# Kernel tuning notes

Hardware: AMD Instinct MI355X
Metric: run time of the kernel (lower is better)

The kernel has to match this reference:

```python
import jax, jax.numpy as jnp
import numpy as np

B, S, HID = 1, 4096, 2048
NH, NKV, HD = 16, 4, 128
BLK, LOCAL, GNB, STRIDE = 64, 4, 2, 4
ROT = 64  # head_dim * rope_partial_rotary_factor(0.5), already even
SCALE = HD ** -0.5
NEG = -1e9


def _block_select(nb):
    """Static local+global key-block selection per query block (mirrors _select_key_blocks)."""
    sels = []
    for bi in range(nb):
        local = list(range(max(0, bi - LOCAL + 1), bi + 1))
        gc = list(range(0, bi + 1, STRIDE))
        if len(gc) > GNB:
            gc = gc[-GNB:]
        if 0 not in gc:
            gc = [0] + gc
        idx = sorted(set(local + gc))
        sels.append([i for i in idx if 0 <= i < nb and i <= bi])
    m = max(len(s) for s in sels)
    idx = np.zeros((nb, m), np.int32)
    valid = np.zeros((nb, m), bool)
    for i, s in enumerate(sels):
        idx[i, :len(s)] = s
        valid[i, :len(s)] = True
    return jnp.asarray(idx), jnp.asarray(valid)


def _rot_half(x):
    h = x.shape[-1] // 2
    return jnp.concatenate([-x[..., h:], x[..., :h]], axis=-1)


def setup_inputs() -> dict:
    key = jax.random.key(0)
    ks = jax.random.split(key, 8)
    w = lambda k, shp: (jax.random.normal(k, shp, jnp.float32) * 0.02)
    return {
        "hidden": jax.random.normal(ks[0], (B, S, HID), jnp.float32),
        "cos": jax.random.uniform(ks[1], (B, S, ROT), jnp.float32, -1.0, 1.0),
        "sin": jax.random.uniform(ks[2], (B, S, ROT), jnp.float32, -1.0, 1.0),
        "Wq": w(ks[3], (HID, NH * HD)),
        "Wk": w(ks[4], (HID, NKV * HD)),
        "Wv": w(ks[5], (HID, NKV * HD)),
        "Wo": w(ks[6], (NH * HD, HID)),
        "attn_mask": jnp.ones((B, S), jnp.float32),
    }


def reference(hidden, cos, sin, Wq, Wk, Wv, Wo, attn_mask):
    b_, s_, _ = hidden.shape
    q = (hidden @ Wq).reshape(b_, s_, NH, HD).transpose(0, 2, 1, 3)   # [B,H,S,d]
    k = (hidden @ Wk).reshape(b_, s_, NKV, HD).transpose(0, 2, 1, 3)  # [B,Hkv,S,d]
    v = (hidden @ Wv).reshape(b_, s_, NKV, HD).transpose(0, 2, 1, 3)

    # partial RoPE on first ROT channels
    c = cos[:, None, :, :]
    sn = sin[:, None, :, :]
    q1, q2 = q[..., :ROT], q[..., ROT:]
    k1, k2 = k[..., :ROT], k[..., ROT:]
    q = jnp.concatenate([q1 * c + _rot_half(q1) * sn, q2], axis=-1)
    k = jnp.concatenate([k1 * c + _rot_half(k1) * sn, k2], axis=-1)

    # repeat_kv (GQA expand: each kv head repeated contiguously)
    rep = NH // NKV
    k = jnp.repeat(k, rep, axis=1)
    v = jnp.repeat(v, rep, axis=1)

    nb = s_ // BLK  # S chosen divisible by BLK (pad_len == 0)
    qb = q.reshape(b_, NH, nb, BLK, HD)
    kb = k.reshape(b_, NH, nb, BLK, HD)
    vb = v.reshape(b_, NH, nb, BLK, HD)

    idx, valid = _block_select(nb)  # [nb, M]
    m = idx.shape[1]
    ksel = kb[:, :, idx]  # [B,H,nb,M,BLK,d]
    vsel = vb[:, :, idx]

    scores = jnp.einsum('bhnqd,bhnmkd->bhnqmk',
                        qb.astype(jnp.float32), ksel.astype(jnp.float32)) * SCALE
    # key-validity (padding) mask, additive as in original
    key_valid = attn_mask.reshape(b_, nb, BLK)
    kvm = key_valid[:, idx]  # [B,nb,M,BLK]
    scores = scores + (1.0 - kvm[:, None, :, None, :, :]) * NEG
    # invalid (padded) selected slots
    scores = jnp.where(valid[None, None, :, None, :, None], scores, NEG)
    # intra-block causal mask on the diagonal block
    intra = jnp.triu(jnp.ones((BLK, BLK), bool), 1)                    # [q,k]
    same = idx == jnp.arange(nb)[:, None]                              # [nb,M]
    diag = same[:, None, :, None] & intra[None, :, None, :]            # [nb,q,M,k]
    scores = jnp.where(diag[None, None], NEG, scores)

    probs = jax.nn.softmax(scores.reshape(b_, NH, nb, BLK, m * BLK), axis=-1)
    vflat = vsel.reshape(b_, NH, nb, m * BLK, HD)
    out = jnp.einsum('bhnqe,bhned->bhnqd', probs.astype(v.dtype), vflat)
    out = out.reshape(b_, NH, s_, HD).transpose(0, 2, 1, 3).reshape(b_, s_, NH * HD)
    return out @ Wo
```

## Files before the change

### kernel.cpp

```cpp
#include <hip/hip_runtime.h>
#include <hip/hip_bf16.h>


typedef short short8 __attribute__((ext_vector_type(8)));
typedef float f32x4 __attribute__((ext_vector_type(4)));

#define NEGV   (-1.0e9f)
#define SCALE  (0.08838834764831845f)

__device__ __forceinline__ void gload16(const void* g, void* l) {
  __builtin_amdgcn_global_load_lds(
      (const __attribute__((address_space(1))) unsigned int*)g,
      (__attribute__((address_space(3))) unsigned int*)l, 16, 0, 0);
}

__device__ __forceinline__ float bf2f(short s) {
  union { unsigned u; float f; } c;
  c.u = ((unsigned)(unsigned short)s) << 16;
  return c.f;
}

__device__ __forceinline__ short f2bf_s(float f) {
  __hip_bfloat16 b = __float2bfloat16(f);
  short s;
  __builtin_memcpy(&s, &b, 2);
  return s;
}

__global__ void conv_hidden(const float* __restrict__ H, __hip_bfloat16* __restrict__ X) {
  size_t t = (size_t)blockIdx.x * 256 + threadIdx.x;
  float4 v = *(const float4*)(H + t * 4);
  __hip_bfloat16* o = X + t * 4;
  o[0] = __float2bfloat16(v.x); o[1] = __float2bfloat16(v.y);
  o[2] = __float2bfloat16(v.z); o[3] = __float2bfloat16(v.w);
}

__global__ void transpose_f32_to_bf16(const float* __restrict__ src,
                                      __hip_bfloat16* __restrict__ dst,
                                      int R, int C) {
  __shared__ __hip_bfloat16 tile[64][73];
  int r0 = blockIdx.x * 64, c0 = blockIdx.y * 64;
  int c = threadIdx.x & 63, rq = threadIdx.x >> 6;
#pragma unroll
  for (int i = 0; i < 16; ++i) {
    int r = i * 4 + rq;
    tile[r][c] = __float2bfloat16(src[(size_t)(r0 + r) * C + c0 + c]);
  }
  __syncthreads();
#pragma unroll
  for (int i = 0; i < 16; ++i) {
    int cc = i * 4 + rq;
    dst[(size_t)(c0 + cc) * R + r0 + c] = tile[c][cc];
  }
}

__global__ void transpose_v(const __hip_bfloat16* __restrict__ QKV,
                            __hip_bfloat16* __restrict__ Vt) {
  __shared__ __hip_bfloat16 tile[64][73];
  int s0 = blockIdx.x * 64, c0 = blockIdx.y * 64;
  int c = threadIdx.x & 63, rq = threadIdx.x >> 6;
#pragma unroll
  for (int i = 0; i < 16; ++i) {
    int r = i * 4 + rq;
    tile[r][c] = QKV[(size_t)(s0 + r) * 3072 + 2560 + c0 + c];
  }
  __syncthreads();
#pragma unroll
  for (int i = 0; i < 16; ++i) {
    int cc = i * 4 + rq;
    Vt[(size_t)(c0 + cc) * 4096 + s0 + c] = tile[c][cc];
  }
}

__global__ void rope_qk(const __hip_bfloat16* __restrict__ QKV, const float* __restrict__ cosb,
                        const float* __restrict__ sinb, __hip_bfloat16* __restrict__ Qb,
                        __hip_bfloat16* __restrict__ Kb) {
  size_t t = (size_t)blockIdx.x * 256 + threadIdx.x;
  const size_t QT = (size_t)4096 * 256;
  int s, cg; const __hip_bfloat16* row; __hip_bfloat16* dst;
  if (t < QT) {
    s = (int)(t >> 8); cg = (int)(t & 255) * 8;
    row = QKV + (size_t)s * 3072;
    dst = Qb + (size_t)s * 2048 + cg;
  } else {
    size_t tk = t - QT;
    s = (int)(tk >> 6); cg = (int)(tk & 63) * 8;
    row = QKV + (size_t)s * 3072 + 2048;
    dst = Kb + (size_t)s * 512 + cg;
  }
  int d = cg & 127;
  short8 v = *(const short8*)(row + cg);
  if (d < 64) {
    short8 p = *(const short8*)(row + cg + (d < 32 ? 32 : -32));
    float sg = (d < 32) ? -1.f : 1.f;
    const float* cp = cosb + (size_t)s * 64 + d;
    const float* sp = sinb + (size_t)s * 64 + d;
    float4 c0 = *(const float4*)cp, c1 = *(const float4*)(cp + 4);
    float4 s0 = *(const float4*)sp, s1 = *(const float4*)(sp + 4);
    float cs[8] = {c0.x, c0.y, c0.z, c0.w, c1.x, c1.y, c1.z, c1.w};
    float sn[8] = {s0.x, s0.y, s0.z, s0.w, s1.x, s1.y, s1.z, s1.w};
    short8 o;
#pragma unroll
    for (int i = 0; i < 8; ++i) {
      float r = bf2f(v[i]) * cs[i] + sg * bf2f(p[i]) * sn[i];
      o[i] = f2bf_s(r);
    }
    *(short8*)dst = o;
  } else {
    *(short8*)dst = v;
  }
}

template <typename OutT>
__global__ __launch_bounds__(256) void gemm_bt(
    const __hip_bfloat16* __restrict__ A, const __hip_bfloat16* __restrict__ Bt,
    OutT* __restrict__ C, int M, int N, int K) {
  const int tid = threadIdx.x;
  const int wave = tid >> 6, lane = tid & 63;
  const int l15 = lane & 15, lg = lane >> 4;
  const int bm = blockIdx.x, bn = blockIdx.y;
  const int wm = wave >> 1, wn = wave & 1;

  __shared__ __hip_bfloat16 As[128 * 64];
  __shared__ __hip_bfloat16 Bs[128 * 64];

  f32x4 acc[4][4] = {};
  const int lrow = lane >> 3;
  const int lslot = lane & 7;
  const int scol = (lslot ^ lrow) * 8;
  const size_t abase = (size_t)bm * 128 * K;
  const size_t bbase = (size_t)bn * 128 * K;
  const int r3 = l15 & 7;

  for (int k0 = 0; k0 < K; k0 += 64) {
#pragma unroll
    for (int i = 0; i < 4; ++i) {
      int seg = i * 4 + wave;
      int row = seg * 8 + lrow;
      gload16(A + abase + (size_t)row * K + k0 + scol, &As[seg * 512]);
      gload16(Bt + bbase + (size_t)row * K + k0 + scol, &Bs[seg * 512]);
    }
    __syncthreads();
#pragma unroll
    for (int ks = 0; ks < 2; ++ks) {
      const int slot = (ks * 4 + lg) ^ r3;
      short8 af[4], bf[4];
#pragma unroll
      for (int mi = 0; mi < 4; ++mi)
        af[mi] = *(const short8*)&As[(wm * 64 + mi * 16 + l15) * 64 + slot * 8];
#pragma unroll
      for (int ni = 0; ni < 4; ++ni)
        bf[ni] = *(const short8*)&Bs[(wn * 64 + ni * 16 + l15) * 64 + slot * 8];
#pragma unroll
      for (int mi = 0; mi < 4; ++mi)
#pragma unroll
        for (int ni = 0; ni < 4; ++ni)
          acc[mi][ni] = __builtin_amdgcn_mfma_f32_16x16x32_bf16(af[mi], bf[ni], acc[mi][ni], 0, 0, 0);
    }
    __syncthreads();
  }
#pragma unroll
  for (int mi = 0; mi < 4; ++mi)
#pragma unroll
    for (int ni = 0; ni < 4; ++ni) {
      int row = bm * 128 + wm * 64 + mi * 16 + lg * 4;
      int col = bn * 128 + wn * 64 + ni * 16 + l15;
#pragma unroll
      for (int r = 0; r < 4; ++r) {
        float v = acc[mi][ni][r];
        if constexpr (__hip_internal::is_same<OutT, float>::value)
          C[(size_t)(row + r) * N + col] = v;
        else
          C[(size_t)(row + r) * N + col] = __float2bfloat16(v);
      }
    }
}

__global__ __launch_bounds__(256, 2) void attn_kernel(
    const __hip_bfloat16* __restrict__ Qb,
    const __hip_bfloat16* __restrict__ Kb,
    const __hip_bfloat16* __restrict__ Vt,
    const float* __restrict__ amask,
    __hip_bfloat16* __restrict__ AO)
{
  const int bid = blockIdx.x;
  const int h = bid & 15;
  const int bi = bid >> 4;
  const int kvh = h >> 2;
  const int tid = threadIdx.x;
  const int wave = tid >> 6, lane = tid & 63;
  const int l15 = lane & 15, lg = lane >> 4;

  int sel[6]; int nsel = 0;
  {
    int gtop = bi >> 2;
    for (int j = 0; j <= bi; ++j) {
      bool pick = (j == 0) || (j >= bi - 3) || (((j & 3) == 0) && ((j >> 2) >= gtop - 1));
      if (pick && nsel < 6) sel[nsel++] = j;
    }
  }

  __shared__ __hip_bfloat16 kvs[128 * 72];
  __shared__ __hip_bfloat16 Pb[64 * 72];

  short8 qf[4];
  {
    const __hip_bfloat16* qbase =
        Qb + (size_t)(bi * 64 + wave * 16 + l15) * 2048 + h * 128 + lg * 8;
#pragma unroll
    for (int ks = 0; ks < 4; ++ks) qf[ks] = *(const short8*)(qbase + ks * 32);
  }

  f32x4 sc[6][4] = {};
#pragma unroll
  for (int j = 0; j < 6; ++j) {
    if (j < nsel) {
      int kb = sel[j];
#pragma unroll
      for (int i = 0; i < 4; ++i) {
        int e = (i * 256 + tid) * 8;
        int r = e >> 7, c = e & 127;
        short8 v = *(const short8*)(Kb + (size_t)(kb * 64 + r) * 512 + kvh * 128 + c);
        *(short8*)&kvs[r * 136 + c] = v;
      }
      __syncthreads();
#pragma unroll
      for (int nf = 0; nf < 4; ++nf)
#pragma unroll
        for (int ks = 0; ks < 4; ++ks) {
          short8 bfr = *(const short8*)&kvs[(nf * 16 + l15) * 136 + ks * 32 + lg * 8];
          sc[j][nf] = __builtin_amdgcn_mfma_f32_16x16x32_bf16(qf[ks], bfr, sc[j][nf], 0, 0, 0);
        }
      __syncthreads();
    }
  }

  float rowmax[4] = {-3.0e38f, -3.0e38f, -3.0e38f, -3.0e38f};
#pragma unroll
  for (int j = 0; j < 6; ++j) {
    if (j >= nsel) continue;
    int kb = sel[j];
#pragma unroll
    for (int nf = 0; nf < 4; ++nf) {
      int keyg = kb * 64 + nf * 16 + l15;
      float mterm = (1.0f - amask[keyg]) * NEGV;
      int keyl = nf * 16 + l15;
#pragma unroll
      for (int r = 0; r < 4; ++r) {
        float s = sc[j][nf][r] * SCALE + mterm;
        if (kb == bi) {
          int qrow = wave * 16 + lg * 4 + r;
          if (keyl > qrow) s = NEGV;
        }
        sc[j][nf][r] = s;
        rowmax[r] = fmaxf(rowmax[r], s);
      }
    }
  }
#pragma unroll
  for (int r = 0; r < 4; ++r) {
    float v = rowmax[r];
    v = fmaxf(v, __shfl_xor(v, 1)); v = fmaxf(v, __shfl_xor(v, 2));
    v = fmaxf(v, __shfl_xor(v, 4)); v = fmaxf(v, __shfl_xor(v, 8));
    rowmax[r] = v;
  }
  float rinv[4] = {0.f, 0.f, 0.f, 0.f};
#pragma unroll
  for (int j = 0; j < 6; ++j) {
    if (j >= nsel) continue;
#pragma unroll
    for (int nf = 0; nf < 4; ++nf)
#pragma unroll
      for (int r = 0; r < 4; ++r) {
        float p = __expf(sc[j][nf][r] - rowmax[r]);
        sc[j][nf][r] = p;
        rinv[r] += p;
      }
  }
#pragma unroll
  for (int r = 0; r < 4; ++r) {
    float v = rinv[r];
    v += __shfl_xor(v, 1); v += __shfl_xor(v, 2);
    v += __shfl_xor(v, 4); v += __shfl_xor(v, 8);
    rinv[r] = 1.0f / v;
  }

  f32x4 oacc[8] = {};
#pragma unroll
  for (int j = 0; j < 6; ++j) {
    if (j < nsel) {
      int kb = sel[j];
#pragma unroll
      for (int nf = 0; nf < 4; ++nf)
#pragma unroll
        for (int r = 0; r < 4; ++r) {
          int qrow = wave * 16 + lg * 4 + r;
          Pb[qrow * 72 + nf * 16 + l15] = __float2bfloat16(sc[j][nf][r] * rinv[r]);
        }
#pragma unroll
      for (int i = 0; i < 4; ++i) {
        int e = (i * 256 + tid) * 8;
        int d = e >> 6, c = e & 63;
        short8 v = *(const short8*)(Vt + (size_t)(kvh * 128 + d) * 4096 + kb * 64 + c);
        *(short8*)&kvs[d * 72 + c] = v;
      }
      __syncthreads();
#pragma unroll
      for (int ks = 0; ks < 2; ++ks) {
        short8 pa = *(const short8*)&Pb[(wave * 16 + l15) * 72 + ks * 32 + lg * 8];
#pragma unroll
        for (int df = 0; df < 8; ++df) {
          short8 vb = *(const short8*)&kvs[(df * 16 + l15) * 72 + ks * 32 + lg * 8];
          oacc[df] = __builtin_amdgcn_mfma_f32_16x16x32_bf16(pa, vb, oacc[df], 0, 0, 0);
        }
      }
      __syncthreads();
    }
  }

#pragma unroll
  for (int df = 0; df < 8; ++df)
#pragma unroll
    for (int r = 0; r < 4; ++r) {
      int qrow = bi * 64 + wave * 16 + lg * 4 + r;
      AO[(size_t)qrow * 2048 + h * 128 + df * 16 + l15] = __float2bfloat16(oacc[df][r]);
    }
}

extern "C" void kernel_launch(void* const* d_in, const int* in_sizes, int n_in,
                              void* d_out, int out_size, void* d_ws, size_t ws_size,
                              hipStream_t stream) {
  const float* hidden = (const float*)d_in[0];
  const float* cosb   = (const float*)d_in[1];
  const float* sinb   = (const float*)d_in[2];
  const float* Wq     = (const float*)d_in[3];
  const float* Wk     = (const float*)d_in[4];
  const float* Wv     = (const float*)d_in[5];
  const float* Wo     = (const float*)d_in[6];
  const float* amask  = (const float*)d_in[7];

  char* ws = (char*)d_ws;
  __hip_bfloat16* Xb   = (__hip_bfloat16*)(ws);
  __hip_bfloat16* Wt   = (__hip_bfloat16*)(ws + 16777216);
  __hip_bfloat16* Wot  = (__hip_bfloat16*)(ws + 29360128);
  __hip_bfloat16* QKVb = (__hip_bfloat16*)(ws + 37748736);
  __hip_bfloat16* Qb   = (__hip_bfloat16*)(ws + 62914560);
  __hip_bfloat16* Kb   = (__hip_bfloat16*)(ws + 79691776);
  __hip_bfloat16* Vt   = (__hip_bfloat16*)(ws + 83886080);
  __hip_bfloat16* AO   = Xb;

  conv_hidden<<<8192, 256, 0, stream>>>(hidden, Xb);
  transpose_f32_to_bf16<<<dim3(32, 32), 256, 0, stream>>>(Wq, Wt, 2048, 2048);
  transpose_f32_to_bf16<<<dim3(32, 8),  256, 0, stream>>>(Wk, Wt + (size_t)2048 * 2048, 2048, 512);
  transpose_f32_to_bf16<<<dim3(32, 8),  256, 0, stream>>>(Wv, Wt + (size_t)2560 * 2048, 2048, 512);
  transpose_f32_to_bf16<<<dim3(32, 32), 256, 0, stream>>>(Wo, Wot, 2048, 2048);

  gemm_bt<__hip_bfloat16><<<dim3(32, 24), 256, 0, stream>>>(Xb, Wt, QKVb, 4096, 3072, 2048);

  rope_qk<<<5120, 256, 0, stream>>>(QKVb, cosb, sinb, Qb, Kb);
  transpose_v<<<dim3(64, 8), 256, 0, stream>>>(QKVb, Vt);

  attn_kernel<<<1024, 256, 0, stream>>>(Qb, Kb, Vt, amask, AO);

  gemm_bt<float><<<dim3(32, 16), 256, 0, stream>>>(AO, Wot, (float*)d_out, 4096, 2048, 2048);
}
```

Measured before the change: 182.0 us.

## Fuse RoPE and V transpose into QKV GEMM epilogue

The QKV projection GEMM now applies partial RoPE to Q and K tiles directly from its accumulators and writes V transposed, so the separate rope_qk and transpose_v kernels and the intermediate QKV buffer go away. This removes two kernel launches and a full write and re-read of the 4096x3072 intermediate. In exchange, the epilogue does strided per-element cos/sin loads and scattered transposed stores from the GEMM. RoPE is also now applied to fp32 accumulators before bf16 rounding, which changes numerics slightly.

```diff
diff --git a/kernel.cpp b/kernel.cpp
--- a/kernel.cpp
+++ b/kernel.cpp
@@ -3,7 +3,8 @@
 
 
 typedef short short8 __attribute__((ext_vector_type(8)));
-typedef float f32x4 __attribute__((ext_vector_type(4)));
+typedef short s16x4  __attribute__((ext_vector_type(4)));
+typedef float f32x4  __attribute__((ext_vector_type(4)));
 
 #define NEGV   (-1.0e9f)
 #define SCALE  (0.08838834764831845f)
@@ -54,67 +55,12 @@
   }
 }
 
-__global__ void transpose_v(const __hip_bfloat16* __restrict__ QKV,
-                            __hip_bfloat16* __restrict__ Vt) {
-  __shared__ __hip_bfloat16 tile[64][73];
-  int s0 = blockIdx.x * 64, c0 = blockIdx.y * 64;
-  int c = threadIdx.x & 63, rq = threadIdx.x >> 6;
-#pragma unroll
-  for (int i = 0; i < 16; ++i) {
-    int r = i * 4 + rq;
-    tile[r][c] = QKV[(size_t)(s0 + r) * 3072 + 2560 + c0 + c];
-  }
-  __syncthreads();
-#pragma unroll
-  for (int i = 0; i < 16; ++i) {
-    int cc = i * 4 + rq;
-    Vt[(size_t)(c0 + cc) * 4096 + s0 + c] = tile[c][cc];
-  }
-}
-
-__global__ void rope_qk(const __hip_bfloat16* __restrict__ QKV, const float* __restrict__ cosb,
-                        const float* __restrict__ sinb, __hip_bfloat16* __restrict__ Qb,
-                        __hip_bfloat16* __restrict__ Kb) {
-  size_t t = (size_t)blockIdx.x * 256 + threadIdx.x;
-  const size_t QT = (size_t)4096 * 256;
-  int s, cg; const __hip_bfloat16* row; __hip_bfloat16* dst;
-  if (t < QT) {
-    s = (int)(t >> 8); cg = (int)(t & 255) * 8;
-    row = QKV + (size_t)s * 3072;
-    dst = Qb + (size_t)s * 2048 + cg;
-  } else {
-    size_t tk = t - QT;
-    s = (int)(tk >> 6); cg = (int)(tk & 63) * 8;
-    row = QKV + (size_t)s * 3072 + 2048;
-    dst = Kb + (size_t)s * 512 + cg;
-  }
-  int d = cg & 127;
-  short8 v = *(const short8*)(row + cg);
-  if (d < 64) {
-    short8 p = *(const short8*)(row + cg + (d < 32 ? 32 : -32));
-    float sg = (d < 32) ? -1.f : 1.f;
-    const float* cp = cosb + (size_t)s * 64 + d;
-    const float* sp = sinb + (size_t)s * 64 + d;
-    float4 c0 = *(const float4*)cp, c1 = *(const float4*)(cp + 4);
-    float4 s0 = *(const float4*)sp, s1 = *(const float4*)(sp + 4);
-    float cs[8] = {c0.x, c0.y, c0.z, c0.w, c1.x, c1.y, c1.z, c1.w};
-    float sn[8] = {s0.x, s0.y, s0.z, s0.w, s1.x, s1.y, s1.z, s1.w};
-    short8 o;
-#pragma unroll
-    for (int i = 0; i < 8; ++i) {
-      float r = bf2f(v[i]) * cs[i] + sg * bf2f(p[i]) * sn[i];
-      o[i] = f2bf_s(r);
-    }
-    *(short8*)dst = o;
-  } else {
-    *(short8*)dst = v;
-  }
-}
-
-template <typename OutT>
-__global__ __launch_bounds__(256) void gemm_bt(
+__global__ __launch_bounds__(256) void gemm_qkv(
     const __hip_bfloat16* __restrict__ A, const __hip_bfloat16* __restrict__ Bt,
-    OutT* __restrict__ C, int M, int N, int K) {
+    const float* __restrict__ cosb, const float* __restrict__ sinb,
+    __hip_bfloat16* __restrict__ Qb, __hip_bfloat16* __restrict__ Kb,
+    __hip_bfloat16* __restrict__ Vt) {
+  const int K = 2048;
   const int tid = threadIdx.x;
   const int wave = tid >> 6, lane = tid & 63;
   const int l15 = lane & 15, lg = lane >> 4;
@@ -159,6 +105,94 @@
     }
     __syncthreads();
   }
+
+  const int srow0 = bm * 128 + wm * 64;
+  if (bn < 20) {
+    __hip_bfloat16* dst; int ld;
+    if (bn < 16) { dst = Qb + (size_t)bn * 128;        ld = 2048; }
+    else         { dst = Kb + (size_t)(bn - 16) * 128; ld = 512;  }
+#pragma unroll
+    for (int mi = 0; mi < 4; ++mi)
+#pragma unroll
+      for (int ni = 0; ni < 4; ++ni) {
+        int dcol = wn * 64 + ni * 16 + l15;
+        int srow = srow0 + mi * 16 + lg * 4;
+#pragma unroll
+        for (int r = 0; r < 4; ++r) {
+          float v = acc[mi][ni][r];
+          if (wn == 0) {
+            int s = srow + r;
+            float cv = cosb[(size_t)s * 64 + dcol];
+            float sv = sinb[(size_t)s * 64 + dcol];
+            float pv = acc[mi][ni ^ 2][r];
+            v = v * cv + (ni < 2 ? -pv : pv) * sv;
+          }
+          dst[(size_t)(srow + r) * ld + dcol] = __float2bfloat16(v);
+        }
+      }
+  } else {
+    const int c0 = (bn - 20) * 128;
+#pragma unroll
+    for (int mi = 0; mi < 4; ++mi)
+#pragma unroll
+      for (int ni = 0; ni < 4; ++ni) {
+        int c  = c0 + wn * 64 + ni * 16 + l15;
+        int s0 = srow0 + mi * 16 + lg * 4;
+        s16x4 o;
+#pragma unroll
+        for (int r = 0; r < 4; ++r) o[r] = f2bf_s(acc[mi][ni][r]);
+        *(s16x4*)&Vt[(size_t)c * 4096 + s0] = o;
+      }
+  }
+}
+
+__global__ __launch_bounds__(256) void gemm_bt(
+    const __hip_bfloat16* __restrict__ A, const __hip_bfloat16* __restrict__ Bt,
+    float* __restrict__ C, int M, int N, int K) {
+  const int tid = threadIdx.x;
+  const int wave = tid >> 6, lane = tid & 63;
+  const int l15 = lane & 15, lg = lane >> 4;
+  const int bm = blockIdx.x, bn = blockIdx.y;
+  const int wm = wave >> 1, wn = wave & 1;
+
+  __shared__ __hip_bfloat16 As[128 * 64];
+  __shared__ __hip_bfloat16 Bs[128 * 64];
+
+  f32x4 acc[4][4] = {};
+  const int lrow = lane >> 3;
+  const int lslot = lane & 7;
+  const int scol = (lslot ^ lrow) * 8;
+  const size_t abase = (size_t)bm * 128 * K;
+  const size_t bbase = (size_t)bn * 128 * K;
+  const int r3 = l15 & 7;
+
+  for (int k0 = 0; k0 < K; k0 += 64) {
+#pragma unroll
+    for (int i = 0; i < 4; ++i) {
+      int seg = i * 4 + wave;
+      int row = seg * 8 + lrow;
+      gload16(A + abase + (size_t)row * K + k0 + scol, &As[seg * 512]);
+      gload16(Bt + bbase + (size_t)row * K + k0 + scol, &Bs[seg * 512]);
+    }
+    __syncthreads();
+#pragma unroll
+    for (int ks = 0; ks < 2; ++ks) {
+      const int slot = (ks * 4 + lg) ^ r3;
+      short8 af[4], bf[4];
+#pragma unroll
+      for (int mi = 0; mi < 4; ++mi)
+        af[mi] = *(const short8*)&As[(wm * 64 + mi * 16 + l15) * 64 + slot * 8];
+#pragma unroll
+      for (int ni = 0; ni < 4; ++ni)
+        bf[ni] = *(const short8*)&Bs[(wn * 64 + ni * 16 + l15) * 64 + slot * 8];
+#pragma unroll
+      for (int mi = 0; mi < 4; ++mi)
+#pragma unroll
+        for (int ni = 0; ni < 4; ++ni)
+          acc[mi][ni] = __builtin_amdgcn_mfma_f32_16x16x32_bf16(af[mi], bf[ni], acc[mi][ni], 0, 0, 0);
+    }
+    __syncthreads();
+  }
 #pragma unroll
   for (int mi = 0; mi < 4; ++mi)
 #pragma unroll
@@ -166,13 +200,8 @@
       int row = bm * 128 + wm * 64 + mi * 16 + lg * 4;
       int col = bn * 128 + wn * 64 + ni * 16 + l15;
 #pragma unroll
-      for (int r = 0; r < 4; ++r) {
-        float v = acc[mi][ni][r];
-        if constexpr (__hip_internal::is_same<OutT, float>::value)
-          C[(size_t)(row + r) * N + col] = v;
-        else
-          C[(size_t)(row + r) * N + col] = __float2bfloat16(v);
-      }
+      for (int r = 0; r < 4; ++r)
+        C[(size_t)(row + r) * N + col] = acc[mi][ni][r];
     }
 }
 
@@ -343,10 +372,9 @@
   __hip_bfloat16* Xb   = (__hip_bfloat16*)(ws);
   __hip_bfloat16* Wt   = (__hip_bfloat16*)(ws + 16777216);
   __hip_bfloat16* Wot  = (__hip_bfloat16*)(ws + 29360128);
-  __hip_bfloat16* QKVb = (__hip_bfloat16*)(ws + 37748736);
-  __hip_bfloat16* Qb   = (__hip_bfloat16*)(ws + 62914560);
-  __hip_bfloat16* Kb   = (__hip_bfloat16*)(ws + 79691776);
-  __hip_bfloat16* Vt   = (__hip_bfloat16*)(ws + 83886080);
+  __hip_bfloat16* Qb   = (__hip_bfloat16*)(ws + 37748736);
+  __hip_bfloat16* Kb   = (__hip_bfloat16*)(ws + 54525952);
+  __hip_bfloat16* Vt   = (__hip_bfloat16*)(ws + 58720256);
   __hip_bfloat16* AO   = Xb;
 
   conv_hidden<<<8192, 256, 0, stream>>>(hidden, Xb);
@@ -355,12 +383,9 @@
   transpose_f32_to_bf16<<<dim3(32, 8),  256, 0, stream>>>(Wv, Wt + (size_t)2560 * 2048, 2048, 512);
   transpose_f32_to_bf16<<<dim3(32, 32), 256, 0, stream>>>(Wo, Wot, 2048, 2048);
 
-  gemm_bt<__hip_bfloat16><<<dim3(32, 24), 256, 0, stream>>>(Xb, Wt, QKVb, 4096, 3072, 2048);
-
-  rope_qk<<<5120, 256, 0, stream>>>(QKVb, cosb, sinb, Qb, Kb);
-  transpose_v<<<dim3(64, 8), 256, 0, stream>>>(QKVb, Vt);
+  gemm_qkv<<<dim3(32, 24), 256, 0, stream>>>(Xb, Wt, cosb, sinb, Qb, Kb, Vt);
 
   attn_kernel<<<1024, 256, 0, stream>>>(Qb, Kb, Vt, amask, AO);
 
-  gemm_bt<float><<<dim3(32, 16), 256, 0, stream>>>(AO, Wot, (float*)d_out, 4096, 2048, 2048);
-}
+  gemm_bt<<<dim3(32, 16), 256, 0, stream>>>(AO, Wot, (float*)d_out, 4096, 2048, 2048);
+}
```

Result: slower. 203.1 us (+11.6%).
